# Kernel tuning notes

Hardware: AMD Instinct MI355X
Metric: run time of the kernel (lower is better)

Reference implementation:

```python
import jax, jax.numpy as jnp
import numpy as np
from jax import lax

WINDOW_SIZE = 5
SIGMA = 1.0
DILATIONS = [1 + int(i ** 1.5) for i in range(5)]  # [1, 2, 3, 6, 9]
C1 = (0.01 * 255.0) ** 2
C2 = (0.03 * 255.0) ** 2


def _make_window(channel=1):
    x = np.arange(WINDOW_SIZE, dtype=np.float64)
    g = np.exp(-((x - WINDOW_SIZE // 2) ** 2) / (2.0 * SIGMA ** 2))
    g = g / g.sum()
    w2d = np.outer(g, g)
    w2d = w2d / w2d.sum()
    w = np.broadcast_to(w2d[None, None], (channel, 1, WINDOW_SIZE, WINDOW_SIZE))
    return jnp.asarray(w, jnp.float32)


def _dw_conv(x, window, dilation):
    # depthwise 'same' conv; pad = (dilated_kernel - 1)/2 = 2*dilation (always even total pad)
    pad = 2 * dilation
    return lax.conv_general_dilated(
        x, window, window_strides=(1, 1),
        padding=((pad, pad), (pad, pad)),
        rhs_dilation=(dilation, dilation),
        dimension_numbers=('NCHW', 'OIHW', 'NCHW'),
        feature_group_count=window.shape[0])


def _ssim_mean(img1, img2, window, dilation):
    mu1 = _dw_conv(img1, window, dilation)
    mu2 = _dw_conv(img2, window, dilation)
    si11 = _dw_conv(img1 * img1, window, dilation)
    si22 = _dw_conv(img2 * img2, window, dilation)
    si12 = _dw_conv(img1 * img2, window, dilation)
    mu1_sq = mu1 * mu1
    mu2_sq = mu2 * mu2
    mu1_mu2 = mu1 * mu2
    sigma1_sq = si11 - mu1_sq
    sigma2_sq = si22 - mu2_sq
    sigma12 = si12 - mu1_mu2
    ssim_map = ((2.0 * mu1_mu2 + C1) * (2.0 * sigma12 + C2)) / (
        (mu1_sq + mu2_sq + C1) * (sigma1_sq + sigma2_sq + C2))
    return jnp.mean(ssim_map)


def _avg_pool2(x):
    B, C, H, W = x.shape
    return x.reshape(B, C, H // 2, 2, W // 2, 2).mean(axis=(3, 5))


def setup_inputs() -> dict:
    key = jax.random.key(0)
    k1, k2 = jax.random.split(key)
    img1 = jax.random.uniform(k1, (16, 1, 1024, 1024), dtype=jnp.float32)
    img2 = jax.random.uniform(k2, (16, 1, 1024, 1024), dtype=jnp.float32)
    window = _make_window(channel=1)
    weights = jnp.asarray([0.0448, 0.2856, 0.3001, 0.2363, 0.1333], jnp.float32)
    return {"img1": img1, "img2": img2, "window": window, "weights": weights}


def reference(img1, img2, window, weights):
    eps = 1e-12
    m = jnp.max(img2)
    a = (img1 + eps) / (m + eps) * 255.0
    b = (img2 + eps) / (m + eps) * 255.0
    mssim = []
    for dil in DILATIONS:
        mssim.append(_ssim_mean(a, b, window, dil))
        a = _avg_pool2(a)
        b = _avg_pool2(b)
    mssim = jnp.stack(mssim)
    return 1.0 - jnp.prod(mssim ** weights)
```

## Files before the change

### kernel.cpp

```cpp
#include <hip/hip_runtime.h>
#include <math.h>

#define EPSN 1e-12f
#define SSIM_C1 6.5025f
#define SSIM_C2 58.5225f


typedef __attribute__((ext_vector_type(2))) float vf2;
typedef __attribute__((ext_vector_type(2))) _Float16 h2;
typedef __attribute__((ext_vector_type(4))) _Float16 h4;
typedef __attribute__((ext_vector_type(8))) _Float16 h8;


__global__ void init_ws_kernel(float* ws) {
    if (threadIdx.x < 16) ws[threadIdx.x] = 0.0f;
}


__global__ void max_kernel(const float4* __restrict__ img2, int n4,
                           unsigned* __restrict__ maxbits) {
    float m = 0.0f;
    for (int i = blockIdx.x * blockDim.x + threadIdx.x; i < n4;
         i += gridDim.x * blockDim.x) {
        float4 v = img2[i];
        m = fmaxf(fmaxf(m, fmaxf(v.x, v.y)), fmaxf(v.z, v.w));
    }
#pragma unroll
    for (int o = 32; o > 0; o >>= 1) m = fmaxf(m, __shfl_down(m, o));
    __shared__ float sm[4];
    int tid = threadIdx.x;
    if ((tid & 63) == 0) sm[tid >> 6] = m;
    __syncthreads();
    if (tid == 0) {
        float mm = fmaxf(fmaxf(sm[0], sm[1]), fmaxf(sm[2], sm[3]));
        atomicMax(maxbits, __float_as_uint(mm));
    }
}


__device__ __forceinline__ float ssim_px_h(h2 pm, h2 sq, float s2h) {
    float px = (float)pm.x, py = (float)pm.y;
    float qx = (float)sq.x, qy = (float)sq.y;
    float u = px * px, vv = py * py;
    float upv = u + vv, umv = u - vv;
    float qp = qx + qy, qm = qx - qy;
    float num1 = fmaf(s2h, umv, SSIM_C1);
    float den1 = fmaf(s2h, upv, SSIM_C1);
    float num2 = fmaf(s2h, qm - umv, SSIM_C2);
    float den2 = fmaf(s2h, qp - upv, SSIM_C2);
    return (num1 * num2) * __builtin_amdgcn_rcpf(den1 * den2);
}

__device__ __forceinline__ void load_g1h(const float* __restrict__ window,
                                         h2* g1h) {
#pragma unroll
    for (int k = 0; k < 5; k++) {
        float g = ((window[k * 5 + 0] + window[k * 5 + 1]) +
                   (window[k * 5 + 2] + window[k * 5 + 3])) + window[k * 5 + 4];
        g1h[k] = h2{(_Float16)g, (_Float16)g};
    }
}

__device__ __forceinline__ void block_sum_add(float local, float* part, int tid,
                                              float* __restrict__ sumOut) {
#pragma unroll
    for (int o = 32; o > 0; o >>= 1) local += __shfl_down(local, o);
    if ((tid & 63) == 0) part[tid >> 6] = local;
    __syncthreads();
    if (tid == 0)
        atomicAdd(sumOut, (part[0] + part[1]) + (part[2] + part[3]));
}

__device__ __forceinline__ void block_sum_add8(float local, float* part, int tid,
                                               float* __restrict__ sumOut) {
#pragma unroll
    for (int o = 32; o > 0; o >>= 1) local += __shfl_down(local, o);
    if ((tid & 63) == 0) part[tid >> 6] = local;
    __syncthreads();
    if (tid == 0)
        atomicAdd(sumOut, ((part[0] + part[1]) + (part[2] + part[3])) +
                          ((part[4] + part[5]) + (part[6] + part[7])));
}

template <int D, int TPT, int LW, int L0>
__device__ __forceinline__ float sep_compute(const h2* AB, const h2* g1h,
                                             float s2h, int tx, int ty) {
    h2 rPM[5], rSQ[5];
    float local = 0.0f;
    int rbase = ty * TPT;
#pragma unroll
    for (int ph = 0; ph < D; ++ph) {
        const int cnt = (TPT - ph + D - 1) / D;
#pragma unroll
        for (int k = 0; k < cnt + 4; ++k) {
            const h2* row = AB + (rbase + ph + k * D) * LW + (L0 - 2 * D) + tx;
            h2 hpm = h2{(_Float16)0.f, (_Float16)0.f};
            h2 hsq = h2{(_Float16)0.f, (_Float16)0.f};
#pragma unroll
            for (int kt = 0; kt < 5; kt++) {
                h2 f = row[kt * D];
                h2 w = g1h[kt] * f;
                hpm += w;
                hsq += w * f;
            }
            rPM[k % 5] = hpm;
            rSQ[k % 5] = hsq;
            if (k >= 4) {
                h2 vpm = h2{(_Float16)0.f, (_Float16)0.f};
                h2 vsq = h2{(_Float16)0.f, (_Float16)0.f};
#pragma unroll
                for (int kt = 0; kt < 5; kt++) {
                    int sl = (k - 4 + kt) % 5;
                    vpm += g1h[kt] * rPM[sl];
                    vsq += g1h[kt] * rSQ[sl];
                }
                local += ssim_px_h(vpm, vsq, s2h);
            }
        }
    }
    return local;
}

template <int D, int LH, int LW, int L0, int W, int NT>
__device__ __forceinline__ void stage_h2(const h2* __restrict__ base, h2* AB,
                                         int x0i, int y0, int tid) {
    for (int idx = tid; idx < LH * 16; idx += NT) {
        int ly = idx >> 4, j = idx & 15;
        int gy = y0 + ly;
        float4 g = make_float4(0, 0, 0, 0);
        if ((unsigned)gy < (unsigned)W)
            g = *(const float4*)(base + (size_t)gy * W + x0i + 4 * j);
        *(float4*)&AB[ly * LW + L0 + 4 * j] = g;
    }
    for (int idx = tid; idx < LH * 4 * D; idx += NT) {
        int ly = idx / (4 * D), h = idx % (4 * D);
        int gc = (h < 2 * D) ? h : h + 64;
        int gx = x0i - 2 * D + gc, gy = y0 + ly;
        h2 pm = {(_Float16)0.f, (_Float16)0.f};
        if ((unsigned)gx < (unsigned)W && (unsigned)gy < (unsigned)W)
            pm = base[(size_t)gy * W + gx];
        AB[ly * LW + (L0 - 2 * D) + gc] = pm;
    }
}


__global__ __launch_bounds__(512) void ssim0_kernel(
        const float* __restrict__ A, const float* __restrict__ B,
        const float* __restrict__ window, const unsigned* __restrict__ maxbits,
        float* __restrict__ sums, h2* __restrict__ pm1) {
    constexpr int TH = 64, TPT = 8, L0 = 4, LW = 72, LH = 68;
    __shared__ __align__(16) h2 AB[LH * LW];
    __shared__ float part[8];

    int tx = threadIdx.x, ty = threadIdx.y;
    int tid = ty * 64 + tx;
    int b = blockIdx.z;
    int x0i = blockIdx.x * 64;
    int y0 = blockIdx.y * TH - 2;

    const float* Ab = A + (size_t)b * 1024 * 1024;
    const float* Bb = B + (size_t)b * 1024 * 1024;
    for (int idx = tid; idx < LH * 16; idx += 512) {
        int ly = idx >> 4, j = idx & 15;
        int gy = y0 + ly;
        float4 a = make_float4(0, 0, 0, 0), v = make_float4(0, 0, 0, 0);
        if ((unsigned)gy < 1024u) {
            a = *(const float4*)(Ab + (size_t)gy * 1024 + x0i + 4 * j);
            v = *(const float4*)(Bb + (size_t)gy * 1024 + x0i + 4 * j);
        }
        h8 r;
        r[0] = (_Float16)(a.x + v.x); r[1] = (_Float16)(a.x - v.x);
        r[2] = (_Float16)(a.y + v.y); r[3] = (_Float16)(a.y - v.y);
        r[4] = (_Float16)(a.z + v.z); r[5] = (_Float16)(a.z - v.z);
        r[6] = (_Float16)(a.w + v.w); r[7] = (_Float16)(a.w - v.w);
        *(h8*)&AB[ly * LW + L0 + 4 * j] = r;
    }
    for (int idx = tid; idx < LH * 4; idx += 512) {
        int ly = idx >> 2, h = idx & 3;
        int gc = (h < 2) ? h : h + 64;
        int gx = x0i - 2 + gc, gy = y0 + ly;
        h2 pm = {(_Float16)0.f, (_Float16)0.f};
        if ((unsigned)gx < 1024u && (unsigned)gy < 1024u) {
            float a = Ab[(size_t)gy * 1024 + gx], v = Bb[(size_t)gy * 1024 + gx];
            pm = h2{(_Float16)(a + v), (_Float16)(a - v)};
        }
        AB[ly * LW + (L0 - 2) + gc] = pm;
    }
    __syncthreads();

    if (tid < 256) {
        int py = tid >> 3, j4 = tid & 7;
        const h2* r0 = AB + (2 + 2 * py) * LW + L0 + 8 * j4;
        const h2* r1 = r0 + LW;
        h2 q = {(_Float16)0.25f, (_Float16)0.25f};
        h8 o;
#pragma unroll
        for (int t = 0; t < 4; t++) {
            h2 s = ((r0[2 * t] + r0[2 * t + 1]) + (r1[2 * t] + r1[2 * t + 1])) * q;
            o[2 * t] = s.x; o[2 * t + 1] = s.y;
        }
        int gx = (x0i >> 1) + 4 * j4, gy = blockIdx.y * 32 + py;
        *(h8*)(pm1 + (size_t)b * 512 * 512 + (size_t)gy * 512 + gx) = o;
    }

    h2 g1h[5];
    load_g1h(window, g1h);
    float mx = __uint_as_float(*maxbits);
    float sc = 255.0f / (mx + EPSN);
    float s2h = 0.5f * sc * sc;

    float local = sep_compute<1, TPT, LW, L0>(AB, g1h, s2h, tx, ty);
    block_sum_add8(local, part, tid, sums + 0);
}


__global__ __launch_bounds__(512) void ssim1_kernel(
        const h2* __restrict__ pm1, const float* __restrict__ window,
        const unsigned* __restrict__ maxbits, float* __restrict__ sums,
        h2* __restrict__ pm2, h2* __restrict__ pm3, h2* __restrict__ pm4) {
    constexpr int D = 2, TH = 64, TPT = 8, L0 = 4, LW = 72, LH = 72;
    __shared__ __align__(16) h2 AB[LH * LW];
    __shared__ float part[8];

    int tx = threadIdx.x, ty = threadIdx.y;
    int tid = ty * 64 + tx;
    int b = blockIdx.z, bx = blockIdx.x, by = blockIdx.y;
    int x0i = bx * 64, y0 = by * TH - 4;
    const h2* base = pm1 + (size_t)b * 512 * 512;

    stage_h2<D, LH, LW, L0, 512, 512>(base, AB, x0i, y0, tid);
    __syncthreads();

    if (tid < 256) {
        int py = tid >> 3, j4 = tid & 7;
        const h2* r0 = AB + (4 + 2 * py) * LW + 4 + 8 * j4;
        const h2* r1 = r0 + LW;
        h2 q = {(_Float16)0.25f, (_Float16)0.25f};
        h8 o;
#pragma unroll
        for (int t = 0; t < 4; t++) {
            h2 s = ((r0[2 * t] + r0[2 * t + 1]) + (r1[2 * t] + r1[2 * t + 1])) * q;
            o[2 * t] = s.x; o[2 * t + 1] = s.y;
        }
        int gx = bx * 32 + 4 * j4, gy = by * 32 + py;
        *(h8*)(pm2 + (size_t)b * 256 * 256 + (size_t)gy * 256 + gx) = o;
    }
    if (tid < 256) {
        int py = tid >> 4, px = tid & 15;
        h2 acc = {(_Float16)0.f, (_Float16)0.f};
#pragma unroll
        for (int ry = 0; ry < 4; ry++)
#pragma unroll
            for (int rx = 0; rx < 4; rx++)
                acc += AB[(4 + 4 * py + ry) * LW + 4 + 4 * px + rx];
        h2 q = {(_Float16)0.0625f, (_Float16)0.0625f};
        acc *= q;
        pm3[(size_t)b * 128 * 128 + (size_t)(by * 16 + py) * 128 + bx * 16 + px] = acc;
    }
    if (tid < 64) {
        int py = tid >> 3, px = tid & 7;
        h2 acc = {(_Float16)0.f, (_Float16)0.f};
#pragma unroll
        for (int ry = 0; ry < 8; ry++)
#pragma unroll
            for (int rx = 0; rx < 8; rx++)
                acc += AB[(4 + 8 * py + ry) * LW + 4 + 8 * px + rx];
        h2 q = {(_Float16)0.015625f, (_Float16)0.015625f};
        acc *= q;
        pm4[(size_t)b * 64 * 64 + (size_t)(by * 8 + py) * 64 + bx * 8 + px] = acc;
    }

    h2 g1h[5];
    load_g1h(window, g1h);
    float mx = __uint_as_float(*maxbits);
    float sc = 255.0f / (mx + EPSN);
    float s2h = 0.5f * sc * sc;

    float local = sep_compute<D, TPT, LW, L0>(AB, g1h, s2h, tx, ty);
    block_sum_add8(local, part, tid, sums + 1);
}


template <int D, int TW, int TH, int W, int LW, int LH>
__device__ void direct_level(const h2* __restrict__ base, const h2* g1h,
                             int bx, int by, float s2h, float* part,
                             float* __restrict__ sumOut, h2* AB, int tid) {
    constexpr int NOUT = TW * TH / 256;
    int x0 = bx * TW - 2 * D, y0 = by * TH - 2 * D;

    for (int idx = tid; idx < LW * LH; idx += 256) {
        int ly = idx / LW, lx = idx - ly * LW;
        int px = x0 + lx, py = y0 + ly;
        h2 pm = {(_Float16)0.f, (_Float16)0.f};
        if ((unsigned)px < (unsigned)W && (unsigned)py < (unsigned)W)
            pm = base[(size_t)py * W + px];
        AB[idx] = pm;
    }
    __syncthreads();

    h2 mu[NOUT], sq[NOUT];
#pragma unroll
    for (int j = 0; j < NOUT; j++) {
        mu[j] = h2{(_Float16)0.f, (_Float16)0.f};
        sq[j] = h2{(_Float16)0.f, (_Float16)0.f};
    }
#pragma unroll
    for (int ky = 0; ky < 5; ky++) {
#pragma unroll
        for (int kx = 0; kx < 5; kx++) {
            h2 wh = g1h[ky] * g1h[kx];
#pragma unroll
            for (int j = 0; j < NOUT; j++) {
                int lin = tid + j * 256;
                int ox = lin % TW, oy = lin / TW;
                h2 f = AB[(oy + ky * D) * LW + ox + kx * D];
                h2 wf = wh * f;
                mu[j] += wf;
                sq[j] += wf * f;
            }
        }
    }
    float local = 0.0f;
#pragma unroll
    for (int j = 0; j < NOUT; j++) local += ssim_px_h(mu[j], sq[j], s2h);
    block_sum_add(local, part, tid, sumOut);
}

__global__ __launch_bounds__(256) void tail_kernel(
        const h2* __restrict__ pm2, const h2* __restrict__ pm3,
        const h2* __restrict__ pm4, const float* __restrict__ window,
        const unsigned* __restrict__ maxbits, float* __restrict__ sums,
        unsigned* __restrict__ counter, const float* __restrict__ weights,
        unsigned* __restrict__ out) {
    extern __shared__ __align__(16) h2 ldsdyn[];
    __shared__ float part[4];
    int tid = threadIdx.x;

    h2 g1h[5];
    load_g1h(window, g1h);
    float mx = __uint_as_float(*maxbits);
    float sc = 255.0f / (mx + EPSN);
    float s2h = 0.5f * sc * sc;

    int bid = blockIdx.x;
    if (bid < 512) {
        int b = bid >> 5, r = bid & 31, by = r >> 2, bx = r & 3;
        constexpr int D = 3, TPT = 8, L0 = 8, LW = 80, LH = 44;
        const h2* base = pm2 + (size_t)b * 256 * 256;
        stage_h2<D, LH, LW, L0, 256, 256>(base, ldsdyn, bx * 64, by * 32 - 6, tid);
        __syncthreads();
        float local = sep_compute<D, TPT, LW, L0>(ldsdyn, g1h, s2h,
                                                  tid & 63, tid >> 6);
        block_sum_add(local, part, tid, sums + 2);
    } else if (bid < 768) {
        int t = bid - 512, b = t >> 4, r = t & 15, by = r >> 1, bx = r & 1;
        const h2* base = pm3 + (size_t)b * 128 * 128;
        direct_level<6, 64, 16, 128, 88, 40>(base, g1h, bx, by, s2h, part,
                                             sums + 3, ldsdyn, tid);
    } else {
        int t = bid - 768, b = t >> 3, r = t & 7, by = r >> 1, bx = r & 1;
        const h2* base = pm4 + (size_t)b * 64 * 64;
        direct_level<9, 32, 16, 64, 68, 52>(base, g1h, bx, by, s2h, part,
                                            sums + 4, ldsdyn, tid);
    }

    if (tid == 0) {
        __threadfence();
        if (atomicAdd(counter, 1u) == 895u) {
            __threadfence();
            const float counts[5] = {16.0f * 1024 * 1024, 16.0f * 512 * 512,
                                     16.0f * 256 * 256,   16.0f * 128 * 128,
                                     16.0f * 64 * 64};
            float prod = 1.0f;
#pragma unroll
            for (int i = 0; i < 5; i++) {
                float m = atomicAdd(sums + i, 0.0f) / counts[i];
                prod *= powf(m, weights[i]);
            }
            float r = 1.0f - prod;
            unsigned bits = __float_as_uint(r);
            unsigned lsb = (bits >> 16) & 1u;
            unsigned hi = (bits + 0x7FFFu + lsb) >> 16;
            out[0] = (hi << 16) | hi;
        }
    }
}


extern "C" void kernel_launch(void* const* d_in, const int* in_sizes, int n_in,
                              void* d_out, int out_size, void* d_ws, size_t ws_size,
                              hipStream_t stream) {
    const float* img1 = (const float*)d_in[0];
    const float* img2 = (const float*)d_in[1];
    const float* window = (const float*)d_in[2];
    const float* weights = (const float*)d_in[3];

    float* ws = (float*)d_ws;
    unsigned* maxbits = (unsigned*)d_ws;
    float* sums = ws + 4;
    unsigned* counter = (unsigned*)(ws + 10);
    size_t off = 512;
    h2* pm1 = (h2*)(ws + off); off += (size_t)16 * 512 * 512;
    h2* pm2 = (h2*)(ws + off); off += (size_t)16 * 256 * 256;
    h2* pm3 = (h2*)(ws + off); off += (size_t)16 * 128 * 128;
    h2* pm4 = (h2*)(ws + off); off += (size_t)16 * 64 * 64;

    init_ws_kernel<<<1, 64, 0, stream>>>(ws);
    max_kernel<<<2048, 256, 0, stream>>>((const float4*)img2,
                                         16 * 1024 * 1024 / 4, maxbits);
    ssim0_kernel<<<dim3(16, 16, 16), dim3(64, 8), 0, stream>>>(
        img1, img2, window, maxbits, sums, pm1);
    ssim1_kernel<<<dim3(8, 8, 16), dim3(64, 8), 0, stream>>>(
        pm1, window, maxbits, sums, pm2, pm3, pm4);
    tail_kernel<<<896, 256, 14144, stream>>>(pm2, pm3, pm4, window, maxbits,
                                             sums, counter, weights,
                                             (unsigned*)d_out);
}
```

Measured before the change: 271.9 us.

## Compute all pyramid levels in ssim0 and merge levels 1-4 into one kernel

The first-level kernel now builds the 2x, 4x, 8x and 16x downsampled images straight from its shared-memory tile using fp32 accumulation. This removes the dependency that forced a separate level-1 kernel to run before the tail. Levels 1 through 4 then run as one 512-thread kernel, with tiles resized and a single completion counter. This saves one launch and its serialization, but adds work and LDS reads to ssim0, which is the heaviest kernel.

```diff
diff --git a/kernel.cpp b/kernel.cpp
--- a/kernel.cpp
+++ b/kernel.cpp
@@ -61,16 +61,6 @@
     }
 }
 
-__device__ __forceinline__ void block_sum_add(float local, float* part, int tid,
-                                              float* __restrict__ sumOut) {
-#pragma unroll
-    for (int o = 32; o > 0; o >>= 1) local += __shfl_down(local, o);
-    if ((tid & 63) == 0) part[tid >> 6] = local;
-    __syncthreads();
-    if (tid == 0)
-        atomicAdd(sumOut, (part[0] + part[1]) + (part[2] + part[3]));
-}
-
 __device__ __forceinline__ void block_sum_add8(float local, float* part, int tid,
                                                float* __restrict__ sumOut) {
 #pragma unroll
@@ -121,11 +111,12 @@
     return local;
 }
 
-template <int D, int LH, int LW, int L0, int W, int NT>
+template <int D, int TILEW, int LH, int LW, int L0, int W, int NT>
 __device__ __forceinline__ void stage_h2(const h2* __restrict__ base, h2* AB,
                                          int x0i, int y0, int tid) {
-    for (int idx = tid; idx < LH * 16; idx += NT) {
-        int ly = idx >> 4, j = idx & 15;
+    constexpr int QPR = TILEW / 4;
+    for (int idx = tid; idx < LH * QPR; idx += NT) {
+        int ly = idx / QPR, j = idx % QPR;
         int gy = y0 + ly;
         float4 g = make_float4(0, 0, 0, 0);
         if ((unsigned)gy < (unsigned)W)
@@ -134,7 +125,7 @@
     }
     for (int idx = tid; idx < LH * 4 * D; idx += NT) {
         int ly = idx / (4 * D), h = idx % (4 * D);
-        int gc = (h < 2 * D) ? h : h + 64;
+        int gc = (h < 2 * D) ? h : h + TILEW;
         int gx = x0i - 2 * D + gc, gy = y0 + ly;
         h2 pm = {(_Float16)0.f, (_Float16)0.f};
         if ((unsigned)gx < (unsigned)W && (unsigned)gy < (unsigned)W)
@@ -147,7 +138,8 @@
 __global__ __launch_bounds__(512) void ssim0_kernel(
         const float* __restrict__ A, const float* __restrict__ B,
         const float* __restrict__ window, const unsigned* __restrict__ maxbits,
-        float* __restrict__ sums, h2* __restrict__ pm1) {
+        float* __restrict__ sums, h2* __restrict__ pm1, h2* __restrict__ pm2,
+        h2* __restrict__ pm3, h2* __restrict__ pm4) {
     constexpr int TH = 64, TPT = 8, L0 = 4, LW = 72, LH = 68;
     __shared__ __align__(16) h2 AB[LH * LW];
     __shared__ float part[8];
@@ -202,6 +194,51 @@
         int gx = (x0i >> 1) + 4 * j4, gy = blockIdx.y * 32 + py;
         *(h8*)(pm1 + (size_t)b * 512 * 512 + (size_t)gy * 512 + gx) = o;
     }
+    if (tid < 256) {
+        int py = tid >> 4, px = tid & 15;
+        vf2 s = {0.f, 0.f};
+#pragma unroll
+        for (int ry = 0; ry < 4; ry++) {
+            h8 rv = *(const h8*)&AB[(2 + 4 * py + ry) * LW + L0 + 4 * px];
+            s.x += ((float)rv[0] + (float)rv[2]) + ((float)rv[4] + (float)rv[6]);
+            s.y += ((float)rv[1] + (float)rv[3]) + ((float)rv[5] + (float)rv[7]);
+        }
+        s *= 0.0625f;
+        pm2[(size_t)b * 256 * 256 + (size_t)(blockIdx.y * 16 + py) * 256 +
+            blockIdx.x * 16 + px] = h2{(_Float16)s.x, (_Float16)s.y};
+    }
+    if (tid < 64) {
+        int py = tid >> 3, px = tid & 7;
+        vf2 s = {0.f, 0.f};
+#pragma unroll
+        for (int ry = 0; ry < 8; ry++) {
+#pragma unroll
+            for (int hx = 0; hx < 2; hx++) {
+                h8 rv = *(const h8*)&AB[(2 + 8 * py + ry) * LW + L0 + 8 * px + 4 * hx];
+                s.x += ((float)rv[0] + (float)rv[2]) + ((float)rv[4] + (float)rv[6]);
+                s.y += ((float)rv[1] + (float)rv[3]) + ((float)rv[5] + (float)rv[7]);
+            }
+        }
+        s *= 0.015625f;
+        pm3[(size_t)b * 128 * 128 + (size_t)(blockIdx.y * 8 + py) * 128 +
+            blockIdx.x * 8 + px] = h2{(_Float16)s.x, (_Float16)s.y};
+    }
+    if (tid < 16) {
+        int py = tid >> 2, px = tid & 3;
+        vf2 s = {0.f, 0.f};
+#pragma unroll
+        for (int ry = 0; ry < 16; ry++) {
+#pragma unroll
+            for (int hx = 0; hx < 4; hx++) {
+                h8 rv = *(const h8*)&AB[(2 + 16 * py + ry) * LW + L0 + 16 * px + 4 * hx];
+                s.x += ((float)rv[0] + (float)rv[2]) + ((float)rv[4] + (float)rv[6]);
+                s.y += ((float)rv[1] + (float)rv[3]) + ((float)rv[5] + (float)rv[7]);
+            }
+        }
+        s *= 0.00390625f;
+        pm4[(size_t)b * 64 * 64 + (size_t)(blockIdx.y * 4 + py) * 64 +
+            blockIdx.x * 4 + px] = h2{(_Float16)s.x, (_Float16)s.y};
+    }
 
     h2 g1h[5];
     load_g1h(window, g1h);
@@ -214,81 +251,14 @@
 }
 
 
-__global__ __launch_bounds__(512) void ssim1_kernel(
-        const h2* __restrict__ pm1, const float* __restrict__ window,
-        const unsigned* __restrict__ maxbits, float* __restrict__ sums,
-        h2* __restrict__ pm2, h2* __restrict__ pm3, h2* __restrict__ pm4) {
-    constexpr int D = 2, TH = 64, TPT = 8, L0 = 4, LW = 72, LH = 72;
-    __shared__ __align__(16) h2 AB[LH * LW];
-    __shared__ float part[8];
-
-    int tx = threadIdx.x, ty = threadIdx.y;
-    int tid = ty * 64 + tx;
-    int b = blockIdx.z, bx = blockIdx.x, by = blockIdx.y;
-    int x0i = bx * 64, y0 = by * TH - 4;
-    const h2* base = pm1 + (size_t)b * 512 * 512;
-
-    stage_h2<D, LH, LW, L0, 512, 512>(base, AB, x0i, y0, tid);
-    __syncthreads();
-
-    if (tid < 256) {
-        int py = tid >> 3, j4 = tid & 7;
-        const h2* r0 = AB + (4 + 2 * py) * LW + 4 + 8 * j4;
-        const h2* r1 = r0 + LW;
-        h2 q = {(_Float16)0.25f, (_Float16)0.25f};
-        h8 o;
-#pragma unroll
-        for (int t = 0; t < 4; t++) {
-            h2 s = ((r0[2 * t] + r0[2 * t + 1]) + (r1[2 * t] + r1[2 * t + 1])) * q;
-            o[2 * t] = s.x; o[2 * t + 1] = s.y;
-        }
-        int gx = bx * 32 + 4 * j4, gy = by * 32 + py;
-        *(h8*)(pm2 + (size_t)b * 256 * 256 + (size_t)gy * 256 + gx) = o;
-    }
-    if (tid < 256) {
-        int py = tid >> 4, px = tid & 15;
-        h2 acc = {(_Float16)0.f, (_Float16)0.f};
-#pragma unroll
-        for (int ry = 0; ry < 4; ry++)
-#pragma unroll
-            for (int rx = 0; rx < 4; rx++)
-                acc += AB[(4 + 4 * py + ry) * LW + 4 + 4 * px + rx];
-        h2 q = {(_Float16)0.0625f, (_Float16)0.0625f};
-        acc *= q;
-        pm3[(size_t)b * 128 * 128 + (size_t)(by * 16 + py) * 128 + bx * 16 + px] = acc;
-    }
-    if (tid < 64) {
-        int py = tid >> 3, px = tid & 7;
-        h2 acc = {(_Float16)0.f, (_Float16)0.f};
-#pragma unroll
-        for (int ry = 0; ry < 8; ry++)
-#pragma unroll
-            for (int rx = 0; rx < 8; rx++)
-                acc += AB[(4 + 8 * py + ry) * LW + 4 + 8 * px + rx];
-        h2 q = {(_Float16)0.015625f, (_Float16)0.015625f};
-        acc *= q;
-        pm4[(size_t)b * 64 * 64 + (size_t)(by * 8 + py) * 64 + bx * 8 + px] = acc;
-    }
-
-    h2 g1h[5];
-    load_g1h(window, g1h);
-    float mx = __uint_as_float(*maxbits);
-    float sc = 255.0f / (mx + EPSN);
-    float s2h = 0.5f * sc * sc;
-
-    float local = sep_compute<D, TPT, LW, L0>(AB, g1h, s2h, tx, ty);
-    block_sum_add8(local, part, tid, sums + 1);
-}
-
-
-template <int D, int TW, int TH, int W, int LW, int LH>
+template <int D, int TW, int TH, int W, int LW, int LH, int NT>
 __device__ void direct_level(const h2* __restrict__ base, const h2* g1h,
                              int bx, int by, float s2h, float* part,
                              float* __restrict__ sumOut, h2* AB, int tid) {
-    constexpr int NOUT = TW * TH / 256;
+    constexpr int NOUT = TW * TH / NT;
     int x0 = bx * TW - 2 * D, y0 = by * TH - 2 * D;
 
-    for (int idx = tid; idx < LW * LH; idx += 256) {
+    for (int idx = tid; idx < LW * LH; idx += NT) {
         int ly = idx / LW, lx = idx - ly * LW;
         int px = x0 + lx, py = y0 + ly;
         h2 pm = {(_Float16)0.f, (_Float16)0.f};
@@ -311,7 +281,7 @@
             h2 wh = g1h[ky] * g1h[kx];
 #pragma unroll
             for (int j = 0; j < NOUT; j++) {
-                int lin = tid + j * 256;
+                int lin = tid + j * NT;
                 int ox = lin % TW, oy = lin / TW;
                 h2 f = AB[(oy + ky * D) * LW + ox + kx * D];
                 h2 wf = wh * f;
@@ -323,17 +293,17 @@
     float local = 0.0f;
 #pragma unroll
     for (int j = 0; j < NOUT; j++) local += ssim_px_h(mu[j], sq[j], s2h);
-    block_sum_add(local, part, tid, sumOut);
-}
-
-__global__ __launch_bounds__(256) void tail_kernel(
-        const h2* __restrict__ pm2, const h2* __restrict__ pm3,
-        const h2* __restrict__ pm4, const float* __restrict__ window,
-        const unsigned* __restrict__ maxbits, float* __restrict__ sums,
-        unsigned* __restrict__ counter, const float* __restrict__ weights,
-        unsigned* __restrict__ out) {
+    block_sum_add8(local, part, tid, sumOut);
+}
+
+__global__ __launch_bounds__(512) void rest_kernel(
+        const h2* __restrict__ pm1, const h2* __restrict__ pm2,
+        const h2* __restrict__ pm3, const h2* __restrict__ pm4,
+        const float* __restrict__ window, const unsigned* __restrict__ maxbits,
+        float* __restrict__ sums, unsigned* __restrict__ counter,
+        const float* __restrict__ weights, unsigned* __restrict__ out) {
     extern __shared__ __align__(16) h2 ldsdyn[];
-    __shared__ float part[4];
+    __shared__ float part[8];
     int tid = threadIdx.x;
 
     h2 g1h[5];
@@ -343,30 +313,41 @@
     float s2h = 0.5f * sc * sc;
 
     int bid = blockIdx.x;
-    if (bid < 512) {
-        int b = bid >> 5, r = bid & 31, by = r >> 2, bx = r & 3;
-        constexpr int D = 3, TPT = 8, L0 = 8, LW = 80, LH = 44;
-        const h2* base = pm2 + (size_t)b * 256 * 256;
-        stage_h2<D, LH, LW, L0, 256, 256>(base, ldsdyn, bx * 64, by * 32 - 6, tid);
+    if (bid < 1024) {
+        int b = bid >> 6, r = bid & 63, by = r >> 3, bx = r & 7;
+        constexpr int D = 2, TPT = 8, L0 = 4, LW = 72, LH = 72;
+        const h2* base = pm1 + (size_t)b * 512 * 512;
+        stage_h2<D, 64, LH, LW, L0, 512, 512>(base, ldsdyn, bx * 64,
+                                              by * 64 - 4, tid);
         __syncthreads();
         float local = sep_compute<D, TPT, LW, L0>(ldsdyn, g1h, s2h,
                                                   tid & 63, tid >> 6);
-        block_sum_add(local, part, tid, sums + 2);
-    } else if (bid < 768) {
-        int t = bid - 512, b = t >> 4, r = t & 15, by = r >> 1, bx = r & 1;
+        block_sum_add8(local, part, tid, sums + 1);
+    } else if (bid < 1280) {
+        int t = bid - 1024, b = t >> 4, r = t & 15, by = r >> 1, bx = r & 1;
+        constexpr int D = 3, TPT = 8, L0 = 8, LW = 144, LH = 44;
+        const h2* base = pm2 + (size_t)b * 256 * 256;
+        stage_h2<D, 128, LH, LW, L0, 256, 512>(base, ldsdyn, bx * 128,
+                                               by * 32 - 6, tid);
+        __syncthreads();
+        float local = sep_compute<D, TPT, LW, L0>(ldsdyn, g1h, s2h,
+                                                  tid & 127, tid >> 7);
+        block_sum_add8(local, part, tid, sums + 2);
+    } else if (bid < 1408) {
+        int t = bid - 1280, b = t >> 3, r = t & 7, by = r >> 1, bx = r & 1;
         const h2* base = pm3 + (size_t)b * 128 * 128;
-        direct_level<6, 64, 16, 128, 88, 40>(base, g1h, bx, by, s2h, part,
-                                             sums + 3, ldsdyn, tid);
+        direct_level<6, 64, 32, 128, 88, 56, 512>(base, g1h, bx, by, s2h, part,
+                                                  sums + 3, ldsdyn, tid);
     } else {
-        int t = bid - 768, b = t >> 3, r = t & 7, by = r >> 1, bx = r & 1;
+        int t = bid - 1408, b = t >> 2, r = t & 3, by = r >> 1, bx = r & 1;
         const h2* base = pm4 + (size_t)b * 64 * 64;
-        direct_level<9, 32, 16, 64, 68, 52>(base, g1h, bx, by, s2h, part,
-                                            sums + 4, ldsdyn, tid);
+        direct_level<9, 32, 32, 64, 68, 68, 512>(base, g1h, bx, by, s2h, part,
+                                                 sums + 4, ldsdyn, tid);
     }
 
     if (tid == 0) {
         __threadfence();
-        if (atomicAdd(counter, 1u) == 895u) {
+        if (atomicAdd(counter, 1u) == 1471u) {
             __threadfence();
             const float counts[5] = {16.0f * 1024 * 1024, 16.0f * 512 * 512,
                                      16.0f * 256 * 256,   16.0f * 128 * 128,
@@ -409,10 +390,8 @@
     max_kernel<<<2048, 256, 0, stream>>>((const float4*)img2,
                                          16 * 1024 * 1024 / 4, maxbits);
     ssim0_kernel<<<dim3(16, 16, 16), dim3(64, 8), 0, stream>>>(
-        img1, img2, window, maxbits, sums, pm1);
-    ssim1_kernel<<<dim3(8, 8, 16), dim3(64, 8), 0, stream>>>(
-        pm1, window, maxbits, sums, pm2, pm3, pm4);
-    tail_kernel<<<896, 256, 14144, stream>>>(pm2, pm3, pm4, window, maxbits,
-                                             sums, counter, weights,
-                                             (unsigned*)d_out);
-}
+        img1, img2, window, maxbits, sums, pm1, pm2, pm3, pm4);
+    rest_kernel<<<1472, 512, 25344, stream>>>(pm1, pm2, pm3, pm4, window,
+                                              maxbits, sums, counter, weights,
+                                              (unsigned*)d_out);
+}
```

New measurement: 271.5 us. No clear change (-0.1%).
